# Kernel optimization log

Hardware: AMD Instinct MI355X
Metric: run time of the kernel (lower is better)

Reference implementation:

```python
import jax, jax.numpy as jnp
import numpy as np

DT = 0.001          # continuous-dynamics step (dt > 0 branch)
KERNEL_SIZE = 16384 # L
P, H = 1024, 256    # d_state, d_input (= d_output)


def setup_inputs() -> dict:
    key = jax.random.key(0)
    kAr, kAi, kB, kC = jax.random.split(key, 4)
    # Continuous diagonal state matrix: real part in [strong, weak] = [-0.5, -0.01] (stable),
    # imaginary part uniform in [-pi, pi] (mimics diagonal_state_space_matrix init).
    Ar = jax.random.uniform(kAr, (P,), minval=-0.5, maxval=-0.01)
    Ai = jax.random.uniform(kAi, (P,), minval=-np.pi, maxval=np.pi)
    A = jnp.stack([Ar, Ai], axis=-1).astype(jnp.float32)            # (P, 2) view_as_real
    # B, C ~ uniform disk (radius 1): scaled complex gaussians are a fine stand-in numerically.
    B = (jax.random.normal(kB, (P, H, 2)) / np.sqrt(H)).astype(jnp.float32)   # (P, H, 2)
    C = (jax.random.normal(kC, (H, P, 2)) / np.sqrt(P)).astype(jnp.float32)   # (H, P, 2)
    return {"A": A, "B": B, "C": C}


def _as_complex(x):
    return x[..., 0] + 1j * x[..., 1]


def reference(A, B, C):
    """Vandermonde SSM kernel generation (continuous dt > 0 branch).
    Returns kernel (H, L, 2) = real view of complex kernel (H, L)."""
    Ac = _as_complex(A)   # (P,) complex
    Bc = _as_complex(B)   # (P, H)
    Cc = _as_complex(C)   # (H, P)

    # ZOH-style discretization
    A_bar = jnp.exp(Ac * DT)                               # (P,)
    B_bar = ((A_bar - 1.0) / Ac)[:, None] * Bc             # (P, H)

    # Vandermonde matrix V[p, l] = A_bar[p] ** l  (complex power == exp(l * log(a)))
    powers = jnp.arange(KERNEL_SIZE, dtype=jnp.float32)    # (L,)
    V = jnp.exp(jnp.log(A_bar)[:, None] * powers[None, :]) # (P, L)

    # W[h, p] = C[h, p] * B_bar[p, h]; kernel[h, l] = sum_p W[h, p] * V[p, l]
    W = Cc * B_bar.T                                       # (H, P)
    kernel = jnp.einsum('hp,pl->hl', W, V)                 # (H, L) complex
    return jnp.stack([kernel.real, kernel.imag], axis=-1)  # (H, L, 2) float32
```

## Files before the change

kernel.cpp:

```cpp
#include <hip/hip_runtime.h>
#include <hip/hip_fp16.h>

#define P_DIM 1024
#define H_DIM 256
#define L_DIM 16384
#define DT 0.001f
#define TWOPI 6.283185307179586f
#define INV2PI 0.15915494309189535f
#define WSCALE 4096.0f
#define INV_WSCALE (1.0f / 4096.0f)
#define BM 128
#define BN 128
#define BK 64
#define NT 256

typedef _Float16 f16x8 __attribute__((ext_vector_type(8)));
typedef float f32x4 __attribute__((ext_vector_type(4)));

#define GPTR(p) (const __attribute__((address_space(1))) unsigned*)(p)
#define LPTR(p) (__attribute__((address_space(3))) unsigned*)(p)

union H2U { __half2 h; unsigned u; };

__device__ __forceinline__ float2 cmulf(float2 a, float2 b) {
    return make_float2(a.x * b.x - a.y * b.y, a.x * b.y + a.y * b.x);
}

__global__ __launch_bounds__(256)
void prep_kernel(const float* __restrict__ Ag, const float* __restrict__ Bg,
                 const float* __restrict__ Cg, __half* __restrict__ W2) {
    __shared__ float2 Bt[64][33];
    __shared__ float2 sc[64];
    const int t  = threadIdx.x;
    const int p0 = (blockIdx.x & 15) << 6;
    const int h0 = (blockIdx.x >> 4) << 5;

    if (t < 64) {
        float2 a = ((const float2*)Ag)[p0 + t];
        float er = __expf(a.x * DT);
        float s, c; __sincosf(a.y * DT, &s, &c);
        float nr = er * c - 1.f, ni = er * s;
        float inv = 1.f / (a.x * a.x + a.y * a.y);
        sc[t] = make_float2((nr * a.x + ni * a.y) * inv, (ni * a.x - nr * a.y) * inv);
    }
    #pragma unroll
    for (int i = 0; i < 8; ++i) {
        int idx = i * 256 + t, p = idx >> 5, h = idx & 31;
        Bt[p][h] = ((const float2*)Bg)[(size_t)(p0 + p) * H_DIM + h0 + h];
    }
    __syncthreads();
    #pragma unroll
    for (int i = 0; i < 8; ++i) {
        int idx = i * 256 + t, h = idx >> 6, p = idx & 63;
        float2 cc = ((const float2*)Cg)[(size_t)(h0 + h) * P_DIM + p0 + p];
        float2 s2 = sc[p], b = Bt[p][h0 ? h : h];
        float2 tv = cmulf(cc, s2);
        float wr = (tv.x * b.x - tv.y * b.y) * WSCALE;
        float wi = (tv.x * b.y + tv.y * b.x) * WSCALE;
        ((__half2*)W2)[(size_t)(h0 + h) * P_DIM + p0 + p] =
            __float22half2_rn(make_float2(wr, wi));
    }
}

__global__ __launch_bounds__(NT, 2)
void vand_mfma_kernel(const float* __restrict__ Ag,
                      const _Float16* __restrict__ W2,
                      float* __restrict__ out) {
    __shared__ __attribute__((aligned(16))) _Float16 As[2][BM * BK];
    __shared__ __attribute__((aligned(16))) _Float16 Bs[2][BN * BK];

    const int tid  = threadIdx.x;
    const int lane = tid & 63;
    const int w    = tid >> 6;
    const int wm   = w & 1, wn = w >> 1;
    const int m0   = blockIdx.y * BM;
    const int nb   = blockIdx.x * BN;
    const int lb   = blockIdx.x * (BN / 2);

    const float2* Ag2 = (const float2*)Ag;

    f32x4 acc[4][4];
    #pragma unroll
    for (int mt = 0; mt < 4; ++mt)
        #pragma unroll
        for (int nt = 0; nt < 4; ++nt)
            acc[mt][nt] = (f32x4){0.f, 0.f, 0.f, 0.f};

    const int q    = tid & 15;
    const int llq  = (tid >> 4) << 2;
    const float l0f = (float)(lb + llq);
    const int grp  = q >> 1, sub = (q & 1) << 2;

    const int goff = (lane >> 3) * 2048 + (((lane & 7) ^ (lane >> 3)) << 3);
    const _Float16* gwbase = W2 + (size_t)(m0 + (w << 5)) * 2048;
    const int ldsoff = (w << 5) * 64;

    _Float16* Acur = &As[0][0]; _Float16* Bcur = &Bs[0][0];
    _Float16* Anxt = &As[1][0]; _Float16* Bnxt = &Bs[1][0];

#define DMA_CHUNK(K0, DST)                                                        \
    {                                                                             \
        const _Float16* gw = gwbase + (K0) + goff;                                \
        _Float16* lB = (DST) + ldsoff;                                            \
        _Pragma("unroll")                                                         \
        for (int r = 0; r < 4; ++r)                                               \
            __builtin_amdgcn_global_load_lds(GPTR(gw + r * 8 * 2048),             \
                                             LPTR(lB + r * 8 * 64), 16, 0, 0);    \
    }

#define VGEN_CHUNK(K0, DST)                                                       \
    {                                                                             \
        float2 a0 = Ag2[((K0) >> 1) + 2 * q];                                     \
        float2 a1 = Ag2[((K0) >> 1) + 2 * q + 1];                                 \
        float c0x = a0.x * DT, c0y = a0.y * (DT * INV2PI);                        \
        float c1x = a1.x * DT, c1y = a1.y * (DT * INV2PI);                        \
        float s, c;                                                               \
        float e0 = __expf(c0x); __sincosf(c0y * TWOPI, &s, &c);                   \
        float2 ab0 = make_float2(e0 * c, e0 * s);                                 \
        float e1 = __expf(c1x); __sincosf(c1y * TWOPI, &s, &c);                   \
        float2 ab1 = make_float2(e1 * c, e1 * s);                                 \
        float mg = __expf(c0x * l0f);                                             \
        float x = c0y * l0f; x -= rintf(x); __sincosf(x * TWOPI, &s, &c);         \
        float2 v0 = make_float2(mg * c, mg * s);                                  \
        mg = __expf(c1x * l0f);                                                   \
        x = c1y * l0f; x -= rintf(x); __sincosf(x * TWOPI, &s, &c);               \
        float2 v1 = make_float2(mg * c, mg * s);                                  \
        _Pragma("unroll")                                                         \
        for (int j = 0; j < 4; ++j) {                                             \
            int n0 = 2 * (llq + j);                                               \
            H2U h0u, h1u, h2u, h3u;                                               \
            h0u.h = __float22half2_rn(make_float2(v0.x, -v0.y));                  \
            h1u.h = __float22half2_rn(make_float2(v1.x, -v1.y));                  \
            h2u.h = __float22half2_rn(make_float2(v0.y, v0.x));                   \
            h3u.h = __float22half2_rn(make_float2(v1.y, v1.x));                   \
            int e0i = n0 * 64 + ((grp ^ (n0 & 7)) << 3) + sub;                    \
            int e1i = (n0 + 1) * 64 + ((grp ^ ((n0 + 1) & 7)) << 3) + sub;        \
            *(uint2*)((DST) + e0i) = make_uint2(h0u.u, h1u.u);                    \
            *(uint2*)((DST) + e1i) = make_uint2(h2u.u, h3u.u);                    \
            if (j < 3) { v0 = cmulf(v0, ab0); v1 = cmulf(v1, ab1); }              \
        }                                                                         \
    }

    DMA_CHUNK(0, Acur)
    VGEN_CHUNK(0, Bcur)
    __syncthreads();

    for (int kk = 0; kk < 32; ++kk) {
        if (kk < 31) {
            const int k1 = (kk + 1) * BK;
            DMA_CHUNK(k1, Anxt)
            VGEN_CHUNK(k1, Bnxt)
        }
        #pragma unroll
        for (int ks = 0; ks < 2; ++ks) {
            f16x8 af[4], bf[4];
            const int g = ks * 4 + (lane >> 4);
            #pragma unroll
            for (int t = 0; t < 4; ++t) {
                int m = wm * 64 + t * 16 + (lane & 15);
                af[t] = *(const f16x8*)(Acur + m * 64 + ((g ^ (m & 7)) << 3));
                int n = wn * 64 + t * 16 + (lane & 15);
                bf[t] = *(const f16x8*)(Bcur + n * 64 + ((g ^ (n & 7)) << 3));
            }
            #pragma unroll
            for (int mt = 0; mt < 4; ++mt)
                #pragma unroll
                for (int nt = 0; nt < 4; ++nt)
                    acc[mt][nt] = __builtin_amdgcn_mfma_f32_16x16x32_f16(
                        af[mt], bf[nt], acc[mt][nt], 0, 0, 0);
        }
        __syncthreads();
        _Float16* tA = Acur; Acur = Anxt; Anxt = tA;
        _Float16* tB = Bcur; Bcur = Bnxt; Bnxt = tB;
    }

    #pragma unroll
    for (int mt = 0; mt < 4; ++mt) {
        #pragma unroll
        for (int nt = 0; nt < 4; ++nt) {
            int h = m0 + wm * 64 + mt * 16 + ((lane >> 4) << 2);
            int n = nb + wn * 64 + nt * 16 + (lane & 15);
            #pragma unroll
            for (int r = 0; r < 4; ++r)
                out[(size_t)(h + r) * 32768 + n] = acc[mt][nt][r] * INV_WSCALE;
        }
    }
#undef DMA_CHUNK
#undef VGEN_CHUNK
}

extern "C" void kernel_launch(void* const* d_in, const int* in_sizes, int n_in,
                              void* d_out, int out_size, void* d_ws, size_t ws_size,
                              hipStream_t stream) {
    const float* A = (const float*)d_in[0];
    const float* B = (const float*)d_in[1];
    const float* C = (const float*)d_in[2];
    float* out = (float*)d_out;
    __half* W2 = (__half*)d_ws;

    prep_kernel<<<dim3(128), dim3(256), 0, stream>>>(A, B, C, W2);
    vand_mfma_kernel<<<dim3(L_DIM * 2 / BN, H_DIM / BM), dim3(NT), 0, stream>>>(
        A, (const _Float16*)W2, out);
}
```

Measured before the change: 111.8 us.

## Fuse W precompute into the GEMM kernel with a grid-wide atomic barrier

Removes the separate prep kernel launch. Each of the 512 GEMM blocks now computes a 512-element slice of the fp16 W matrix, then all blocks wait on a global atomic-counter barrier before the MFMA main loop. This saves one kernel launch and the gap between launches. In exchange it adds a spin barrier that needs all 512 blocks to be resident at once, which holds only if 2 blocks per CU fit across the 256 CUs. A bounded spin budget stops a hang but could let a block read stale W if the barrier times out.

```diff
diff --git a/kernel.cpp b/kernel.cpp
--- a/kernel.cpp
+++ b/kernel.cpp
@@ -8,7 +8,7 @@
 #define TWOPI 6.283185307179586f
 #define INV2PI 0.15915494309189535f
 #define WSCALE 4096.0f
-#define INV_WSCALE (1.0f / 4096.0f)
+#define INVS (1.0f / 4096.0f)
 #define BM 128
 #define BN 128
 #define BK 64
@@ -26,46 +26,12 @@
     return make_float2(a.x * b.x - a.y * b.y, a.x * b.y + a.y * b.x);
 }
 
-__global__ __launch_bounds__(256)
-void prep_kernel(const float* __restrict__ Ag, const float* __restrict__ Bg,
-                 const float* __restrict__ Cg, __half* __restrict__ W2) {
-    __shared__ float2 Bt[64][33];
-    __shared__ float2 sc[64];
-    const int t  = threadIdx.x;
-    const int p0 = (blockIdx.x & 15) << 6;
-    const int h0 = (blockIdx.x >> 4) << 5;
-
-    if (t < 64) {
-        float2 a = ((const float2*)Ag)[p0 + t];
-        float er = __expf(a.x * DT);
-        float s, c; __sincosf(a.y * DT, &s, &c);
-        float nr = er * c - 1.f, ni = er * s;
-        float inv = 1.f / (a.x * a.x + a.y * a.y);
-        sc[t] = make_float2((nr * a.x + ni * a.y) * inv, (ni * a.x - nr * a.y) * inv);
-    }
-    #pragma unroll
-    for (int i = 0; i < 8; ++i) {
-        int idx = i * 256 + t, p = idx >> 5, h = idx & 31;
-        Bt[p][h] = ((const float2*)Bg)[(size_t)(p0 + p) * H_DIM + h0 + h];
-    }
-    __syncthreads();
-    #pragma unroll
-    for (int i = 0; i < 8; ++i) {
-        int idx = i * 256 + t, h = idx >> 6, p = idx & 63;
-        float2 cc = ((const float2*)Cg)[(size_t)(h0 + h) * P_DIM + p0 + p];
-        float2 s2 = sc[p], b = Bt[p][h0 ? h : h];
-        float2 tv = cmulf(cc, s2);
-        float wr = (tv.x * b.x - tv.y * b.y) * WSCALE;
-        float wi = (tv.x * b.y + tv.y * b.x) * WSCALE;
-        ((__half2*)W2)[(size_t)(h0 + h) * P_DIM + p0 + p] =
-            __float22half2_rn(make_float2(wr, wi));
-    }
-}
+__device__ unsigned g_ctr = 0;
 
 __global__ __launch_bounds__(NT, 2)
-void vand_mfma_kernel(const float* __restrict__ Ag,
-                      const _Float16* __restrict__ W2,
-                      float* __restrict__ out) {
+void vand_one(const float* __restrict__ Ag, const float* __restrict__ Bg,
+              const float* __restrict__ Cg, __half* __restrict__ W2,
+              float* __restrict__ out) {
     __shared__ __attribute__((aligned(16))) _Float16 As[2][BM * BK];
     __shared__ __attribute__((aligned(16))) _Float16 Bs[2][BN * BK];
 
@@ -79,6 +45,42 @@
 
     const float2* Ag2 = (const float2*)Ag;
 
+    {
+        const int blk = blockIdx.y * gridDim.x + blockIdx.x;
+        const float2* B2 = (const float2*)Bg;
+        const float2* C2 = (const float2*)Cg;
+        #pragma unroll
+        for (int i = 0; i < 2; ++i) {
+            int e = blk * 512 + i * 256 + tid;
+            int h = e >> 10, p = e & 1023;
+            float2 a = Ag2[p];
+            float er = __expf(a.x * DT);
+            float s, c;
+            __sincosf(a.y * DT, &s, &c);
+            float nr = er * c - 1.0f, ni = er * s;
+            float inv = 1.0f / (a.x * a.x + a.y * a.y);
+            float sr = (nr * a.x + ni * a.y) * inv;
+            float si = (ni * a.x - nr * a.y) * inv;
+            float2 b  = B2[(size_t)p * H_DIM + h];
+            float2 cc = C2[(size_t)h * P_DIM + p];
+            float tr = cc.x * sr - cc.y * si, ti = cc.x * si + cc.y * sr;
+            float wr = (tr * b.x - ti * b.y) * WSCALE;
+            float wi = (tr * b.y + ti * b.x) * WSCALE;
+            ((__half2*)W2)[e] = __float22half2_rn(make_float2(wr, wi));
+        }
+    }
+    __threadfence();
+    if (tid == 0) {
+        unsigned old = atomicAdd(&g_ctr, 1u);
+        unsigned tgt = (old - (old & 511u)) + 512u;
+        unsigned budget = 2000000u;
+        while (atomicAdd(&g_ctr, 0u) < tgt && --budget) {
+            __builtin_amdgcn_s_sleep(8);
+        }
+    }
+    __syncthreads();
+    __threadfence();
+
     f32x4 acc[4][4];
     #pragma unroll
     for (int mt = 0; mt < 4; ++mt)
@@ -92,7 +94,7 @@
     const int grp  = q >> 1, sub = (q & 1) << 2;
 
     const int goff = (lane >> 3) * 2048 + (((lane & 7) ^ (lane >> 3)) << 3);
-    const _Float16* gwbase = W2 + (size_t)(m0 + (w << 5)) * 2048;
+    const _Float16* gwbase = (const _Float16*)W2 + (size_t)(m0 + (w << 5)) * 2048;
     const int ldsoff = (w << 5) * 64;
 
     _Float16* Acur = &As[0][0]; _Float16* Bcur = &Bs[0][0];
@@ -182,7 +184,7 @@
             int n = nb + wn * 64 + nt * 16 + (lane & 15);
             #pragma unroll
             for (int r = 0; r < 4; ++r)
-                out[(size_t)(h + r) * 32768 + n] = acc[mt][nt][r] * INV_WSCALE;
+                out[(size_t)(h + r) * 32768 + n] = acc[mt][nt][r] * INVS;
         }
     }
 #undef DMA_CHUNK
@@ -198,7 +200,6 @@
     float* out = (float*)d_out;
     __half* W2 = (__half*)d_ws;
 
-    prep_kernel<<<dim3(128), dim3(256), 0, stream>>>(A, B, C, W2);
-    vand_mfma_kernel<<<dim3(L_DIM * 2 / BN, H_DIM / BM), dim3(NT), 0, stream>>>(
-        A, (const _Float16*)W2, out);
+    vand_one<<<dim3(L_DIM * 2 / BN, H_DIM / BM), dim3(NT), 0, stream>>>(
+        A, B, C, W2, out);
 }
```

Measured after the change: 188.6 us. +68.7%, slower.
